# Kernel tuning notes

Measured on AMD Instinct MI355X. Metric: run time of the kernel, lower is better.

Reference implementation:

```python
import jax, jax.numpy as jnp
import numpy as np

N_TREES = 100
N_TRAIN = 40000
N_QUERY = 1024
N_LEAVES = 512
EPS = 1e-8


def setup_inputs() -> dict:
    key = jax.random.key(0)
    k1, k2 = jax.random.split(key)
    # Per-tree leaf id of each query point: equivalent of tree.apply(X) per tree.
    query_leaf_ids = jax.random.randint(k1, (N_TREES, N_QUERY), 0, N_LEAVES, dtype=jnp.int32)
    # Per-tree leaf id of each training point: equivalent of tree.apply(X_train).
    train_leaf_ids = jax.random.randint(k2, (N_TREES, N_TRAIN), 0, N_LEAVES, dtype=jnp.int32)
    # Uniform vote weight per tree (original sums unit counts then divides by T).
    tree_weights = jnp.ones((N_TREES,), dtype=jnp.float32)
    return {
        "tree_weights": tree_weights,
        "query_leaf_ids": query_leaf_ids,
        "train_leaf_ids": train_leaf_ids,
    }


def reference(tree_weights, query_leaf_ids, train_leaf_ids):
    # weights[m, j] = (1/T) * sum_t tw[t] * 1[leaf_t(query m) == leaf_t(train j)]
    T = tree_weights.shape[0]
    M = query_leaf_ids.shape[1]
    n_train = train_leaf_ids.shape[1]

    def step(acc, inputs):
        tw, q_leaf, tr_leaf = inputs  # scalar, [M], [n_train]
        # Co-membership indicator for this tree: [M, n_train]
        ind = (q_leaf[:, None] == tr_leaf[None, :]).astype(acc.dtype)
        return acc + tw * ind, None

    init = jnp.zeros((M, n_train), dtype=jnp.float32)
    weights, _ = jax.lax.scan(step, init, (tree_weights, query_leaf_ids, train_leaf_ids))
    weights = weights / T  # average over trees
    # Row-normalize so each query's weights sum to 1 (with eps, as in original).
    weights = weights / (jnp.sum(weights, axis=1, keepdims=True) + EPS)
    return weights
```

## Files before the change

kernel.cpp:

```cpp
#include <hip/hip_runtime.h>
#include <hip/hip_bf16.h>
#include <stdint.h>

#define N_TREES  100
#define N_TRAIN  40000
#define N_QUERY  1024
#define N_LEAVES 512
#define HALF_J   (N_TRAIN / 2)
#define HALF_W   (HALF_J / 4)
#define QUART_J  (N_TRAIN / 4)
#define PADQ     13584
#define NVT      200

#define BIDX_BYTES ((size_t)N_TREES * 4 * PADQ * 2)
#define BPK_OFF    BIDX_BYTES
#define BPK_BYTES  ((size_t)N_TREES * 4 * N_LEAVES * 4)
#define WS_NEEDED  (BPK_OFF + BPK_BYTES)

__global__ __launch_bounds__(256) void build_part(const int* __restrict__ train,
                                                  uint32_t* __restrict__ bpk,
                                                  uint16_t* __restrict__ bidx) {
    const int t    = blockIdx.x >> 2;
    const int part = blockIdx.x & 3;
    const int tid  = threadIdx.x;
    __shared__ __align__(16) uint16_t stage[PADQ];
    __shared__ uint32_t hist[N_LEAVES];
    __shared__ uint32_t sbuf[2][N_LEAVES];
    __shared__ uint32_t cursor[N_LEAVES];
    __shared__ uint32_t totpad_sh;

    hist[tid] = 0;
    hist[tid + 256] = 0;
    __syncthreads();

    const int4* tr4 = (const int4*)(train + t * N_TRAIN + part * QUART_J);
    for (int i = tid; i < QUART_J / 4; i += 256) {
        int4 v = tr4[i];
        atomicAdd(&hist[v.x], 1u);
        atomicAdd(&hist[v.y], 1u);
        atomicAdd(&hist[v.z], 1u);
        atomicAdd(&hist[v.w], 1u);
    }
    __syncthreads();

    const uint32_t len0 = hist[tid], len1 = hist[tid + 256];
    sbuf[0][tid]       = (len0 + 7u) & ~7u;
    sbuf[0][tid + 256] = (len1 + 7u) & ~7u;
    __syncthreads();
    int src = 0;
    for (int d = 1; d < N_LEAVES; d <<= 1) {
        uint32_t a = sbuf[src][tid]       + ((tid >= d)       ? sbuf[src][tid - d]       : 0u);
        uint32_t b = sbuf[src][tid + 256] + ((tid + 256 >= d) ? sbuf[src][tid + 256 - d] : 0u);
        sbuf[src ^ 1][tid]       = a;
        sbuf[src ^ 1][tid + 256] = b;
        __syncthreads();
        src ^= 1;
    }
    {
        const uint32_t start0 = sbuf[src][tid]       - ((len0 + 7u) & ~7u);
        const uint32_t start1 = sbuf[src][tid + 256] - ((len1 + 7u) & ~7u);
        uint32_t* bp = bpk + (size_t)(t * 4 + part) * N_LEAVES;
        bp[tid]       = (len0 << 16) | start0;
        bp[tid + 256] = (len1 << 16) | start1;
        cursor[tid]       = start0;
        cursor[tid + 256] = start1;
        if (tid == 255) totpad_sh = sbuf[src][N_LEAVES - 1];
    }
    __syncthreads();

    for (int i = tid; i < QUART_J / 4; i += 256) {
        int4 v = tr4[i];
        const int j = part * QUART_J + i * 4;
        uint32_t p0 = atomicAdd(&cursor[v.x], 1u); stage[p0] = (uint16_t)j;
        uint32_t p1 = atomicAdd(&cursor[v.y], 1u); stage[p1] = (uint16_t)(j + 1);
        uint32_t p2 = atomicAdd(&cursor[v.z], 1u); stage[p2] = (uint16_t)(j + 2);
        uint32_t p3 = atomicAdd(&cursor[v.w], 1u); stage[p3] = (uint16_t)(j + 3);
    }
    __syncthreads();

    const uint32_t n16 = totpad_sh >> 3;
    const uint4* s4 = (const uint4*)stage;
    uint4* g4 = (uint4*)(bidx + (size_t)(t * 4 + part) * PADQ);
    for (uint32_t i = tid; i < n16; i += 256) g4[i] = s4[i];
}

__global__ __launch_bounds__(256) void row_kernel(const int* __restrict__ qleaf,
                                                  const uint16_t* __restrict__ bidx,
                                                  const uint32_t* __restrict__ bpk,
                                                  float* __restrict__ out) {
    const int m    = blockIdx.x >> 1;
    const int half = blockIdx.x & 1;
    const int jlo  = half * HALF_J;
    const int tid  = threadIdx.x;
    __shared__ __align__(16) uint32_t cnt[HALF_W];
    __shared__ uint16_t su[NVT];
    __shared__ uint16_t lu[NVT];
    __shared__ uint16_t treetot[N_TREES + 28];
    __shared__ uint16_t cpref[NVT + 1];
    __shared__ float    inv_sh;

    uint4* c4 = (uint4*)cnt;
    for (int i = tid; i < HALF_W / 4; i += 256) c4[i] = make_uint4(0, 0, 0, 0);
    if (tid < N_TREES + 28) treetot[tid] = 0;
    __syncthreads();
    if (tid < N_TREES) {
        const int q = qleaf[tid * N_QUERY + m];
        const uint32_t* bp = bpk + (size_t)tid * 4 * N_LEAVES + q;
        const uint32_t pk0 = bp[(2 * half)     * N_LEAVES];
        const uint32_t pk1 = bp[(2 * half + 1) * N_LEAVES];
        const uint32_t po0 = bp[(2 * (half ^ 1))     * N_LEAVES];
        const uint32_t po1 = bp[(2 * (half ^ 1) + 1) * N_LEAVES];
        su[2 * tid]     = (uint16_t)(pk0 & 0xffffu);
        su[2 * tid + 1] = (uint16_t)(pk1 & 0xffffu);
        lu[2 * tid]     = (uint16_t)(pk0 >> 16);
        lu[2 * tid + 1] = (uint16_t)(pk1 >> 16);
        treetot[tid] = (uint16_t)((pk0 >> 16) + (pk1 >> 16) + (po0 >> 16) + (po1 >> 16));
    }
    __syncthreads();

    if (tid < 64) {
        uint32_t e[4], s = 0;
        #pragma unroll
        for (int k = 0; k < 4; ++k) {
            const int idx = 4 * tid + k;
            const uint32_t c = (idx < NVT) ? ((uint32_t)(lu[idx] + 7u) >> 3) : 0u;
            e[k] = s; s += c;
        }
        uint32_t inc = s;
        for (int o = 1; o < 64; o <<= 1) {
            uint32_t v = __shfl_up(inc, o, 64);
            if (tid >= o) inc += v;
        }
        const uint32_t excl = inc - s;
        #pragma unroll
        for (int k = 0; k < 4; ++k) {
            const int idx = 4 * tid + k;
            if (idx <= NVT) cpref[idx] = (uint16_t)(excl + e[k]);
        }
        uint32_t tot = (uint32_t)treetot[tid] + (uint32_t)treetot[tid + 64];
        for (int o = 32; o > 0; o >>= 1) tot += __shfl_down(tot, o, 64);
        if (tid == 0) inv_sh = 1.0f / ((float)tot + 1e-6f);
    }
    __syncthreads();

    const int Ctot = cpref[NVT];
    for (int c = tid; c < Ctot; c += 256) {
        int vt = 0;
        #pragma unroll
        for (int step = 128; step >= 1; step >>= 1) {
            const int cand = vt + step;
            if (cand <= NVT - 1 && (int)cpref[cand] <= c) vt = cand;
        }
        const int cc  = c - (int)cpref[vt];
        const int rem = (int)lu[vt] - cc * 8;
        const int n   = rem > 8 ? 8 : rem;
        const int tt  = vt >> 1, sub = vt & 1;
        const uint4 w = *(const uint4*)(bidx +
            (size_t)(tt * 4 + 2 * half + sub) * PADQ + su[vt] + cc * 8);
        uint32_t e[8] = { w.x & 0xffffu, w.x >> 16, w.y & 0xffffu, w.y >> 16,
                          w.z & 0xffffu, w.z >> 16, w.w & 0xffffu, w.w >> 16 };
        #pragma unroll
        for (int i = 0; i < 8; ++i)
            if (i < n) {
                const uint32_t lj = e[i] - (uint32_t)jlo;
                atomicAdd(&cnt[lj >> 2], 1u << ((lj & 3u) * 8u));
            }
    }
    __syncthreads();

    const float inv = inv_sh;
    float4* orow = (float4*)(out + (size_t)m * N_TRAIN + jlo);
    for (int p = tid; p < HALF_W; p += 256) {
        const uint32_t w = cnt[p];
        float4 v;
        v.x = (float)(w & 0xffu) * inv;
        v.y = (float)((w >> 8) & 0xffu) * inv;
        v.z = (float)((w >> 16) & 0xffu) * inv;
        v.w = (float)(w >> 24) * inv;
        orow[p] = v;
    }
}

__global__ __launch_bounds__(1024) void row_kernel_direct(const int* __restrict__ qleaf,
                                                          const int* __restrict__ train,
                                                          float* __restrict__ out) {
    const int m   = blockIdx.x;
    const int tid = threadIdx.x;
    __shared__ uint32_t cnt[N_TRAIN / 2];
    __shared__ int      qlds[N_TREES];
    __shared__ uint32_t total_sh;

    if (tid < N_TREES) qlds[tid] = qleaf[tid * N_QUERY + m];
    if (tid == 0) total_sh = 0;
    __syncthreads();

    const int2* tr2 = (const int2*)train;
    for (int p = tid; p < N_TRAIN / 2; p += 1024) {
        uint32_t c0 = 0, c1 = 0;
        for (int t = 0; t < N_TREES; ++t) {
            const int q = qlds[t];
            int2 v = tr2[t * (N_TRAIN / 2) + p];
            c0 += (v.x == q);
            c1 += (v.y == q);
        }
        cnt[p] = c0 | (c1 << 16);
    }
    __syncthreads();

    uint32_t local = 0;
    for (int p = tid; p < N_TRAIN / 2; p += 1024) {
        uint32_t w = cnt[p];
        local += (w & 0xffffu) + (w >> 16);
    }
    const int lane = tid & 63;
    for (int o = 32; o > 0; o >>= 1) local += __shfl_down(local, o, 64);
    if (lane == 0) atomicAdd(&total_sh, local);
    __syncthreads();

    const float inv = 1.0f / ((float)total_sh + 1e-6f);
    float2* orow = (float2*)(out + (size_t)m * N_TRAIN);
    for (int p = tid; p < N_TRAIN / 2; p += 1024) {
        uint32_t w = cnt[p];
        float2 v;
        v.x = (float)(w & 0xffffu) * inv;
        v.y = (float)(w >> 16) * inv;
        orow[p] = v;
    }
}

extern "C" void kernel_launch(void* const* d_in, const int* in_sizes, int n_in,
                              void* d_out, int out_size, void* d_ws, size_t ws_size,
                              hipStream_t stream) {
    const int* qleaf = (const int*)d_in[1];
    const int* train = (const int*)d_in[2];
    float* out = (float*)d_out;

    if (ws_size >= WS_NEEDED) {
        uint16_t* bidx = (uint16_t*)d_ws;
        uint32_t* bpk  = (uint32_t*)((char*)d_ws + BPK_OFF);
        build_part<<<N_TREES * 4, 256, 0, stream>>>(train, bpk, bidx);
        row_kernel<<<N_QUERY * 2, 256, 0, stream>>>(qleaf, bidx, bpk, out);
    } else {
        row_kernel_direct<<<N_QUERY, 1024, 0, stream>>>(qleaf, train, out);
    }
}
```

Baseline: 53.54 us.

## Split each query row across four blocks and interleave bucket metadata per leaf

```diff
diff --git a/kernel.cpp b/kernel.cpp
--- a/kernel.cpp
+++ b/kernel.cpp
@@ -6,15 +6,13 @@
 #define N_TRAIN  40000
 #define N_QUERY  1024
 #define N_LEAVES 512
-#define HALF_J   (N_TRAIN / 2)
-#define HALF_W   (HALF_J / 4)
 #define QUART_J  (N_TRAIN / 4)
+#define QUART_W  (QUART_J / 4)
 #define PADQ     13584
-#define NVT      200
 
 #define BIDX_BYTES ((size_t)N_TREES * 4 * PADQ * 2)
 #define BPK_OFF    BIDX_BYTES
-#define BPK_BYTES  ((size_t)N_TREES * 4 * N_LEAVES * 4)
+#define BPK_BYTES  ((size_t)N_TREES * N_LEAVES * 4 * 4)
 #define WS_NEEDED  (BPK_OFF + BPK_BYTES)
 
 __global__ __launch_bounds__(256) void build_part(const int* __restrict__ train,
@@ -59,9 +57,9 @@
     {
         const uint32_t start0 = sbuf[src][tid]       - ((len0 + 7u) & ~7u);
         const uint32_t start1 = sbuf[src][tid + 256] - ((len1 + 7u) & ~7u);
-        uint32_t* bp = bpk + (size_t)(t * 4 + part) * N_LEAVES;
-        bp[tid]       = (len0 << 16) | start0;
-        bp[tid + 256] = (len1 << 16) | start1;
+        uint32_t* bp = bpk + (size_t)t * N_LEAVES * 4 + part;
+        bp[(size_t)tid * 4]         = (len0 << 16) | start0;
+        bp[(size_t)(tid + 256) * 4] = (len1 << 16) | start1;
         cursor[tid]       = start0;
         cursor[tid + 256] = start1;
         if (tid == 255) totpad_sh = sbuf[src][N_LEAVES - 1];
@@ -88,75 +86,67 @@
                                                   const uint16_t* __restrict__ bidx,
                                                   const uint32_t* __restrict__ bpk,
                                                   float* __restrict__ out) {
-    const int m    = blockIdx.x >> 1;
-    const int half = blockIdx.x & 1;
-    const int jlo  = half * HALF_J;
+    const int m    = blockIdx.x >> 2;
+    const int part = blockIdx.x & 3;
+    const int jlo  = part * QUART_J;
     const int tid  = threadIdx.x;
-    __shared__ __align__(16) uint32_t cnt[HALF_W];
-    __shared__ uint16_t su[NVT];
-    __shared__ uint16_t lu[NVT];
+    __shared__ __align__(16) uint32_t cnt[QUART_W];
+    __shared__ uint16_t su[N_TREES];
+    __shared__ uint16_t lu[N_TREES];
     __shared__ uint16_t treetot[N_TREES + 28];
-    __shared__ uint16_t cpref[NVT + 1];
+    __shared__ uint16_t cpref[N_TREES + 1];
     __shared__ float    inv_sh;
 
     uint4* c4 = (uint4*)cnt;
-    for (int i = tid; i < HALF_W / 4; i += 256) c4[i] = make_uint4(0, 0, 0, 0);
+    for (int i = tid; i < QUART_W / 4; i += 256) c4[i] = make_uint4(0, 0, 0, 0);
     if (tid < N_TREES + 28) treetot[tid] = 0;
     __syncthreads();
     if (tid < N_TREES) {
         const int q = qleaf[tid * N_QUERY + m];
-        const uint32_t* bp = bpk + (size_t)tid * 4 * N_LEAVES + q;
-        const uint32_t pk0 = bp[(2 * half)     * N_LEAVES];
-        const uint32_t pk1 = bp[(2 * half + 1) * N_LEAVES];
-        const uint32_t po0 = bp[(2 * (half ^ 1))     * N_LEAVES];
-        const uint32_t po1 = bp[(2 * (half ^ 1) + 1) * N_LEAVES];
-        su[2 * tid]     = (uint16_t)(pk0 & 0xffffu);
-        su[2 * tid + 1] = (uint16_t)(pk1 & 0xffffu);
-        lu[2 * tid]     = (uint16_t)(pk0 >> 16);
-        lu[2 * tid + 1] = (uint16_t)(pk1 >> 16);
-        treetot[tid] = (uint16_t)((pk0 >> 16) + (pk1 >> 16) + (po0 >> 16) + (po1 >> 16));
+        const uint4 pk4 = *(const uint4*)(bpk + ((size_t)tid * N_LEAVES + q) * 4);
+        const uint32_t own = (part == 0) ? pk4.x : (part == 1) ? pk4.y
+                           : (part == 2) ? pk4.z : pk4.w;
+        su[tid] = (uint16_t)(own & 0xffffu);
+        lu[tid] = (uint16_t)(own >> 16);
+        treetot[tid] = (uint16_t)((pk4.x >> 16) + (pk4.y >> 16) +
+                                  (pk4.z >> 16) + (pk4.w >> 16));
     }
     __syncthreads();
 
     if (tid < 64) {
-        uint32_t e[4], s = 0;
-        #pragma unroll
-        for (int k = 0; k < 4; ++k) {
-            const int idx = 4 * tid + k;
-            const uint32_t c = (idx < NVT) ? ((uint32_t)(lu[idx] + 7u) >> 3) : 0u;
-            e[k] = s; s += c;
-        }
+        const int i0 = 2 * tid, i1 = 2 * tid + 1;
+        const uint32_t l0 = (i0 < N_TREES) ? lu[i0] : 0u;
+        const uint32_t l1 = (i1 < N_TREES) ? lu[i1] : 0u;
+        const uint32_t c0 = (l0 + 7u) >> 3, c1 = (l1 + 7u) >> 3;
+        const uint32_t s  = c0 + c1;
         uint32_t inc = s;
         for (int o = 1; o < 64; o <<= 1) {
             uint32_t v = __shfl_up(inc, o, 64);
             if (tid >= o) inc += v;
         }
         const uint32_t excl = inc - s;
-        #pragma unroll
-        for (int k = 0; k < 4; ++k) {
-            const int idx = 4 * tid + k;
-            if (idx <= NVT) cpref[idx] = (uint16_t)(excl + e[k]);
-        }
+        if (i0 <= N_TREES) cpref[i0] = (uint16_t)excl;
+        if (i1 <= N_TREES) cpref[i1] = (uint16_t)(excl + c0);
+        if (tid == 63) cpref[N_TREES] = (uint16_t)inc;
         uint32_t tot = (uint32_t)treetot[tid] + (uint32_t)treetot[tid + 64];
         for (int o = 32; o > 0; o >>= 1) tot += __shfl_down(tot, o, 64);
         if (tid == 0) inv_sh = 1.0f / ((float)tot + 1e-6f);
     }
     __syncthreads();
 
-    const int Ctot = cpref[NVT];
+    const int Ctot = cpref[N_TREES];
     for (int c = tid; c < Ctot; c += 256) {
-        int vt = 0;
+        int t = 0;
         #pragma unroll
-        for (int step = 128; step >= 1; step >>= 1) {
-            const int cand = vt + step;
-            if (cand <= NVT - 1 && (int)cpref[cand] <= c) vt = cand;
+        for (int step = 64; step >= 1; step >>= 1) {
+            const int cand = t + step;
+            if (cand <= N_TREES - 1 && (int)cpref[cand] <= c) t = cand;
         }
-        const int cc  = c - (int)cpref[vt];
-        const int rem = (int)lu[vt] - cc * 8;
+        const int cc  = c - (int)cpref[t];
+        const int rem = (int)lu[t] - cc * 8;
         const int n   = rem > 8 ? 8 : rem;
-        const int tt  = vt >> 1, sub = vt & 1;
         const uint4 w = *(const uint4*)(bidx +
-            (size_t)(tt * 4 + 2 * half + sub) * PADQ + su[vt] + cc * 8);
+            (size_t)(t * 4 + part) * PADQ + su[t] + cc * 8);
         uint32_t e[8] = { w.x & 0xffffu, w.x >> 16, w.y & 0xffffu, w.y >> 16,
                           w.z & 0xffffu, w.z >> 16, w.w & 0xffffu, w.w >> 16 };
         #pragma unroll
@@ -170,7 +160,7 @@
 
     const float inv = inv_sh;
     float4* orow = (float4*)(out + (size_t)m * N_TRAIN + jlo);
-    for (int p = tid; p < HALF_W; p += 256) {
+    for (int p = tid; p < QUART_W; p += 256) {
         const uint32_t w = cnt[p];
         float4 v;
         v.x = (float)(w & 0xffu) * inv;
@@ -239,7 +229,7 @@
         uint16_t* bidx = (uint16_t*)d_ws;
         uint32_t* bpk  = (uint32_t*)((char*)d_ws + BPK_OFF);
         build_part<<<N_TREES * 4, 256, 0, stream>>>(train, bpk, bidx);
-        row_kernel<<<N_QUERY * 2, 256, 0, stream>>>(qleaf, bidx, bpk, out);
+        row_kernel<<<N_QUERY * 4, 256, 0, stream>>>(qleaf, bidx, bpk, out);
     } else {
         row_kernel_direct<<<N_QUERY, 1024, 0, stream>>>(qleaf, train, out);
     }
```

After: 49.92 us, median of 3. -6.8%, faster.
